# Performance work log

Hardware: AMD Instinct MI355X
Metric: run time of the kernel (lower is better)

Reference implementation:

```python
import jax, jax.numpy as jnp
import numpy as np

B, IN, H, OUT = 256, 512, 1024, 512
S, Wd, SH = 512, 256, 3          # memory_slots, memory_width, shift_range
P_READ = Wd + 2 + SH + 1         # key, beta, gate, shift(3), gamma
P_WRITE = P_READ + 2 * Wd        # + erase, add


def setup_inputs() -> dict:
    key = jax.random.key(0)
    ks = jax.random.split(key, 8)
    sc = 0.02
    return {
        "x": jax.random.normal(ks[0], (B, IN), jnp.float32),
        "W_ih": jax.random.normal(ks[1], (4 * H, IN + Wd), jnp.float32) * sc,
        "b_ih": jnp.zeros((4 * H,), jnp.float32),
        "W_hh": jax.random.normal(ks[2], (4 * H, H), jnp.float32) * sc,
        "b_hh": jnp.zeros((4 * H,), jnp.float32),
        "W_read": jax.random.normal(ks[3], (P_READ, H), jnp.float32) * sc,
        "b_read": jnp.zeros((P_READ,), jnp.float32),
        "W_write": jax.random.normal(ks[4], (P_WRITE, H), jnp.float32) * sc,
        "b_write": jnp.zeros((P_WRITE,), jnp.float32),
        "W_out": jax.random.normal(ks[5], (OUT, H + Wd), jnp.float32) * sc,
        "b_out": jnp.zeros((OUT,), jnp.float32),
        "mem_bias": jax.random.normal(ks[6], (S, Wd), jnp.float32) * sc,
    }


def _content_address(key_v, beta, memory):
    # cosine similarity of key [B,Wd] vs memory [B,S,Wd], eps=1e-8 like torch
    num = jnp.einsum('bw,bsw->bs', key_v, memory)
    kn = jnp.maximum(jnp.linalg.norm(key_v, axis=1, keepdims=True), 1e-8)
    mn = jnp.maximum(jnp.linalg.norm(memory, axis=2), 1e-8)
    sim = num / (kn * mn) * beta[:, None]
    return jax.nn.softmax(sim, axis=1)


def _address(p, prev_w, memory):
    # content_and_location addressing for a single head
    key_v = p[:, :Wd]
    beta = jax.nn.softplus(p[:, Wd])
    gate = jax.nn.sigmoid(p[:, Wd + 1])
    shift = jax.nn.softmax(p[:, Wd + 2:Wd + 2 + SH], axis=1)
    gamma = 1.0 + jax.nn.softplus(p[:, Wd + 2 + SH])
    cw = _content_address(key_v, beta, memory)
    g = gate[:, None]
    gw = g * cw + (1.0 - g) * prev_w  # interpolation gate
    # circular shift: shifted[pos] = s0*w[pos-1] + s1*w[pos] + s2*w[pos+1]
    sw = (shift[:, 0:1] * jnp.roll(gw, 1, axis=1)
          + shift[:, 1:2] * gw
          + shift[:, 2:3] * jnp.roll(gw, -1, axis=1))
    sp = sw ** gamma[:, None]  # sharpening
    return sp / (jnp.sum(sp, axis=1, keepdims=True) + 1e-6)


def reference(x, W_ih, b_ih, W_hh, b_hh, W_read, b_read, W_write, b_write, W_out, b_out, mem_bias):
    Bb = x.shape[0]
    # init_state (prev_state=None path)
    memory = jnp.broadcast_to(mem_bias[None], (Bb, S, Wd))
    w0 = jnp.zeros((Bb, S), x.dtype).at[:, 0].set(1.0)
    rv = jnp.zeros((Bb, Wd), x.dtype)
    h = jnp.zeros((Bb, H), x.dtype)
    c = jnp.zeros((Bb, H), x.dtype)
    # LSTMCell controller
    inp = jnp.concatenate([x, rv], axis=1)
    gates = inp @ W_ih.T + b_ih + h @ W_hh.T + b_hh
    i, f, g, o = jnp.split(gates, 4, axis=1)
    c = jax.nn.sigmoid(f) * c + jax.nn.sigmoid(i) * jnp.tanh(g)
    h = jax.nn.sigmoid(o) * jnp.tanh(c)
    # read head addressing (1 head)
    rp = h @ W_read.T + b_read
    read_w = _address(rp, w0, memory)
    # write head addressing + erase/add (1 head)
    wp = h @ W_write.T + b_write
    write_w = _address(wp, w0, memory)
    erase = jax.nn.sigmoid(wp[:, P_READ:P_READ + Wd])
    add = jnp.tanh(wp[:, P_READ + Wd:])
    memory = memory * (1.0 - write_w[:, :, None] * erase[:, None, :]) + write_w[:, :, None] * add[:, None, :]
    # read after write
    rv = jnp.einsum('bsw,bs->bw', memory, read_w)
    out = jnp.concatenate([h, rv], axis=1) @ W_out.T + b_out
    return out
```

## Files before the change

### kernel.cpp

```cpp
#include <hip/hip_runtime.h>
#include <hip/hip_bf16.h>
#include <math.h>

#define BB   256
#define INW  512
#define HH   1024
#define OUTW 512
#define SS   512
#define WD   256
#define P_READ  262
#define P_WRITE 774
#define RW_LD   1056
#define W_OFF   272

typedef __attribute__((ext_vector_type(8))) short bf16x8;
typedef __attribute__((ext_vector_type(4))) float f32x4;

__device__ __forceinline__ float sigmoidf(float x) { return 1.f / (1.f + expf(-x)); }
__device__ __forceinline__ float softplusf(float x) { return (x > 20.f) ? x : log1pf(expf(x)); }
__device__ __forceinline__ unsigned short f2b(float f) {
    union { float f; unsigned u; } c; c.f = f;
    return (unsigned short)((c.u + 0x7FFFu + ((c.u >> 16) & 1u)) >> 16);
}
__device__ __forceinline__ void st_bf4(__hip_bfloat16* d, float a, float b, float c, float e) {
    ushort4 u; u.x = f2b(a); u.y = f2b(b); u.z = f2b(c); u.w = f2b(e);
    *reinterpret_cast<ushort4*>(d) = u;
}
__device__ __forceinline__ float wave_sum(float v) {
    #pragma unroll
    for (int off = 32; off > 0; off >>= 1) v += __shfl_down(v, off, 64);
    return v;
}

#define N_WIH (3072*512)
#define N_WRW (RW_LD*1024)
#define N_WO  (512*1280)
#define N_X   (256*512)
#define N_MB  (512*256)
#define N_MT  (256*512)
#define N_BIA 3072
#define N_BRW RW_LD
#define N_TOT (N_WIH+N_WRW+N_WO+N_X+N_MB+N_MT+N_BIA+N_BRW)
#define NB_CVT ((N_TOT/4 + 255) / 256)

__global__ __launch_bounds__(256)
void convert_all(const float* __restrict__ W_ih, const float* __restrict__ b_ih,
                 const float* __restrict__ b_hh,
                 const float* __restrict__ W_read, const float* __restrict__ b_read,
                 const float* __restrict__ W_write, const float* __restrict__ b_write,
                 const float* __restrict__ W_out, const float* __restrict__ x,
                 const float* __restrict__ mem,
                 __hip_bfloat16* __restrict__ Wih_c, __hip_bfloat16* __restrict__ Wrw_p,
                 __hip_bfloat16* __restrict__ Wo_b, __hip_bfloat16* __restrict__ x_b,
                 __hip_bfloat16* __restrict__ mem_b, __hip_bfloat16* __restrict__ memT_b,
                 float* __restrict__ bias_c, float* __restrict__ bias_rw,
                 float* __restrict__ mem_norm)
{
    if (blockIdx.x >= NB_CVT) {
        __shared__ float red[4];
        int s = blockIdx.x - NB_CVT;
        float v = mem[(size_t)s * WD + threadIdx.x];
        float vv = wave_sum(v * v);
        if ((threadIdx.x & 63) == 0) red[threadIdx.x >> 6] = vv;
        __syncthreads();
        if (threadIdx.x == 0)
            mem_norm[s] = fmaxf(sqrtf(red[0] + red[1] + red[2] + red[3]), 1e-8f);
        return;
    }
    long i = ((long)blockIdx.x * 256 + threadIdx.x) * 4;
    if (i >= N_TOT) return;
    if (i < N_WIH) {
        int r = (int)(i >> 9), c = (int)(i & 511);
        int sr = r < 1024 ? r : r + 1024;
        float4 v = *reinterpret_cast<const float4*>(W_ih + (size_t)sr * 768 + c);
        st_bf4(Wih_c + i, v.x, v.y, v.z, v.w);
        return;
    }
    i -= N_WIH;
    if (i < N_WRW) {
        int r = (int)(i >> 10), c = (int)(i & 1023);
        float4 v = make_float4(0.f, 0.f, 0.f, 0.f);
        if (r < W_OFF) { if (r < P_READ) v = *reinterpret_cast<const float4*>(W_read + (size_t)r * 1024 + c); }
        else { int wr = r - W_OFF; if (wr < P_WRITE) v = *reinterpret_cast<const float4*>(W_write + (size_t)wr * 1024 + c); }
        st_bf4(Wrw_p + i, v.x, v.y, v.z, v.w);
        return;
    }
    i -= N_WRW;
    if (i < N_WO) {
        float4 v = *reinterpret_cast<const float4*>(W_out + i);
        st_bf4(Wo_b + i, v.x, v.y, v.z, v.w);
        return;
    }
    i -= N_WO;
    if (i < N_X) {
        float4 v = *reinterpret_cast<const float4*>(x + i);
        st_bf4(x_b + i, v.x, v.y, v.z, v.w);
        return;
    }
    i -= N_X;
    if (i < N_MB) {
        float4 v = *reinterpret_cast<const float4*>(mem + i);
        st_bf4(mem_b + i, v.x, v.y, v.z, v.w);
        return;
    }
    i -= N_MB;
    if (i < N_MT) {
        int w = (int)(i >> 9), s = (int)(i & 511);
        st_bf4(memT_b + i, mem[(size_t)s * 256 + w], mem[(size_t)(s + 1) * 256 + w],
               mem[(size_t)(s + 2) * 256 + w], mem[(size_t)(s + 3) * 256 + w]);
        return;
    }
    i -= N_MT;
    if (i < N_BIA) {
        #pragma unroll
        for (int u = 0; u < 4; ++u) {
            long r = i + u;
            long sr = r < 1024 ? r : r + 1024;
            bias_c[r] = b_ih[sr] + b_hh[sr];
        }
        return;
    }
    i -= N_BIA;
    {
        #pragma unroll
        for (int u = 0; u < 4; ++u) {
            long r = i + u;
            float v = 0.f;
            if (r < W_OFF) { if (r < P_READ) v = b_read[r]; }
            else { long wr = r - W_OFF; if (wr < P_WRITE) v = b_write[wr]; }
            bias_rw[r] = v;
        }
    }
}

__global__ __launch_bounds__(64)
void gemm_gates(const __hip_bfloat16* __restrict__ x_b,
                const __hip_bfloat16* __restrict__ Wih_c,
                const float* __restrict__ bias_c,
                __hip_bfloat16* __restrict__ h_b)
{
    const int l = threadIdx.x;
    const int bn = blockIdx.x * 16;
    const int bm = blockIdx.y * 16;
    const int r = l & 15, q = l >> 4;
    const __hip_bfloat16* ap = x_b + (size_t)(bm + r) * INW + q * 8;
    const __hip_bfloat16* bi = Wih_c + (size_t)(bn + r) * INW + q * 8;
    const __hip_bfloat16* bg = bi + (size_t)1024 * INW;
    const __hip_bfloat16* bo = bi + (size_t)2048 * INW;
    f32x4 ai = {0.f,0.f,0.f,0.f}, ag = ai, ao = ai;
    #pragma unroll
    for (int k = 0; k < INW; k += 32) {
        bf16x8 a = *reinterpret_cast<const bf16x8*>(ap + k);
        ai = __builtin_amdgcn_mfma_f32_16x16x32_bf16(a, *reinterpret_cast<const bf16x8*>(bi + k), ai, 0, 0, 0);
        ag = __builtin_amdgcn_mfma_f32_16x16x32_bf16(a, *reinterpret_cast<const bf16x8*>(bg + k), ag, 0, 0, 0);
        ao = __builtin_amdgcn_mfma_f32_16x16x32_bf16(a, *reinterpret_cast<const bf16x8*>(bo + k), ao, 0, 0, 0);
    }
    const int j = bn + r;
    const float bii = bias_c[j], big = bias_c[1024 + j], bio = bias_c[2048 + j];
    #pragma unroll
    for (int jj = 0; jj < 4; ++jj) {
        int b = bm + q * 4 + jj;
        float c = sigmoidf(ai[jj] + bii) * tanhf(ag[jj] + big);
        h_b[(size_t)b * HH + j] = __float2bfloat16(sigmoidf(ao[jj] + bio) * tanhf(c));
    }
}

__global__ __launch_bounds__(64)
void gemm_dual(const __hip_bfloat16* __restrict__ h_b,
               const __hip_bfloat16* __restrict__ Wrw_p,
               const __hip_bfloat16* __restrict__ Wo_b,
               const float* __restrict__ bias_rw, const float* __restrict__ b_out,
               float* __restrict__ rpwp, float* __restrict__ out,
               __hip_bfloat16* __restrict__ keys)
{
    const int bid = blockIdx.x;
    const int lane = threadIdx.x;
    const int r = lane & 15, q = lane >> 4;
    int bm, bn, ldb;
    const __hip_bfloat16* B;
    if (bid < 1056) { int nt = bid % 66, mt = bid / 66; bm = mt * 16; bn = nt * 16; B = Wrw_p; ldb = HH; }
    else { int o = bid - 1056; int nt = o & 31, mt = o >> 5; bm = mt * 16; bn = nt * 16; B = Wo_b; ldb = 1280; }

    const __hip_bfloat16* ap = h_b + (size_t)(bm + r) * HH + q * 8;
    const __hip_bfloat16* bp = B + (size_t)(bn + r) * ldb + q * 8;
    f32x4 a0 = {0.f,0.f,0.f,0.f}, a1 = a0;
    #pragma unroll 8
    for (int k = 0; k < 512; k += 32) {
        a0 = __builtin_amdgcn_mfma_f32_16x16x32_bf16(
            *reinterpret_cast<const bf16x8*>(ap + k),
            *reinterpret_cast<const bf16x8*>(bp + k), a0, 0, 0, 0);
        a1 = __builtin_amdgcn_mfma_f32_16x16x32_bf16(
            *reinterpret_cast<const bf16x8*>(ap + 512 + k),
            *reinterpret_cast<const bf16x8*>(bp + 512 + k), a1, 0, 0, 0);
    }
    const int col = bn + r;
    if (bid < 1056) {
        const float bv = bias_rw[col];
        #pragma unroll
        for (int j = 0; j < 4; ++j) {
            int m = bm + q * 4 + j;
            float v = a0[j] + a1[j] + bv;
            rpwp[(size_t)m * RW_LD + col] = v;
            if (col < WD)
                keys[(size_t)m * WD + col] = __float2bfloat16(v);
            else if (col >= W_OFF && col < W_OFF + WD)
                keys[(size_t)(256 + m) * WD + (col - W_OFF)] = __float2bfloat16(v);
        }
    } else {
        const float bv = b_out[col];
        #pragma unroll
        for (int j = 0; j < 4; ++j) {
            int m = bm + q * 4 + j;
            out[(size_t)m * OUTW + col] = a0[j] + a1[j] + bv;
        }
    }
}

__global__ __launch_bounds__(64)
void gemm_num(const __hip_bfloat16* __restrict__ keys,
              const __hip_bfloat16* __restrict__ mem_b,
              const float* __restrict__ mem_norm,
              float* __restrict__ numd)
{
    const int l = threadIdx.x;
    const int bn = blockIdx.x * 16;
    const int bm = blockIdx.y * 16;
    const int r = l & 15, q = l >> 4;
    const __hip_bfloat16* ap = keys + (size_t)(bm + r) * WD + q * 8;
    const __hip_bfloat16* bp = mem_b + (size_t)(bn + r) * WD + q * 8;
    f32x4 acc = {0.f,0.f,0.f,0.f};
    #pragma unroll
    for (int k = 0; k < WD; k += 32)
        acc = __builtin_amdgcn_mfma_f32_16x16x32_bf16(
            *reinterpret_cast<const bf16x8*>(ap + k),
            *reinterpret_cast<const bf16x8*>(bp + k), acc, 0, 0, 0);
    const int col = bn + r;
    const float inv = 1.f / mem_norm[col];
    #pragma unroll
    for (int j = 0; j < 4; ++j)
        numd[(size_t)(bm + q * 4 + j) * SS + col] = acc[j] * inv;
}

__device__ __forceinline__ void redpair_sum(float& a, float& b, volatile float* redA, volatile float* redB) {
    #pragma unroll
    for (int off = 32; off > 0; off >>= 1) { a += __shfl_down(a, off, 64); b += __shfl_down(b, off, 64); }
    int wid = threadIdx.x >> 6;
    __syncthreads();
    if ((threadIdx.x & 63) == 0) { redA[wid] = a; redB[wid] = b; }
    __syncthreads();
    a = redA[0]+redA[1]+redA[2]+redA[3]+redA[4]+redA[5]+redA[6]+redA[7];
    b = redB[0]+redB[1]+redB[2]+redB[3]+redB[4]+redB[5]+redB[6]+redB[7];
}
__device__ __forceinline__ void redpair_max(float& a, float& b, volatile float* redA, volatile float* redB) {
    #pragma unroll
    for (int off = 32; off > 0; off >>= 1) { a = fmaxf(a, __shfl_down(a, off, 64)); b = fmaxf(b, __shfl_down(b, off, 64)); }
    int wid = threadIdx.x >> 6;
    __syncthreads();
    if ((threadIdx.x & 63) == 0) { redA[wid] = a; redB[wid] = b; }
    __syncthreads();
    a = fmaxf(fmaxf(fmaxf(redA[0],redA[1]),fmaxf(redA[2],redA[3])),fmaxf(fmaxf(redA[4],redA[5]),fmaxf(redA[6],redA[7])));
    b = fmaxf(fmaxf(fmaxf(redB[0],redB[1]),fmaxf(redB[2],redB[3])),fmaxf(fmaxf(redB[4],redB[5]),fmaxf(redB[6],redB[7])));
}

__global__ __launch_bounds__(512)
void address_fused(const float* __restrict__ rpwp, const float* __restrict__ numd,
                   __hip_bfloat16* __restrict__ A12, float* __restrict__ t3)
{
    const int b = blockIdx.x;
    const int t = threadIdx.x;
    const float* pr = rpwp + (size_t)b * RW_LD;
    const float* pw = pr + W_OFF;

    __shared__ float redA[8], redB[8];
    __shared__ float bufr[SS], bufw[SS];

    float beta_r  = softplusf(pr[WD]);
    float gate_r  = sigmoidf(pr[WD + 1]);
    float r0 = pr[WD+2], r1 = pr[WD+3], r2 = pr[WD+4];
    float rmx = fmaxf(r0, fmaxf(r1, r2));
    float re0 = expf(r0-rmx), re1 = expf(r1-rmx), re2 = expf(r2-rmx);
    float rinv = 1.f / (re0+re1+re2);
    float shr0 = re0*rinv, shr1 = re1*rinv, shr2 = re2*rinv;
    float gamma_r = 1.f + softplusf(pr[WD + 5]);

    float beta_w  = softplusf(pw[WD]);
    float gate_w  = sigmoidf(pw[WD + 1]);
    float w0 = pw[WD+2], w1 = pw[WD+3], w2 = pw[WD+4];
    float wmx = fmaxf(w0, fmaxf(w1, w2));
    float we0 = expf(w0-wmx), we1 = expf(w1-wmx), we2 = expf(w2-wmx);
    float winv = 1.f / (we0+we1+we2);
    float shw0 = we0*winv, shw1 = we1*winv, shw2 = we2*winv;
    float gamma_w = 1.f + softplusf(pw[WD + 5]);

    {
        float kv = (t < WD) ? pr[t] : pw[t - WD];
        float vv = kv * kv;
        #pragma unroll
        for (int off = 32; off > 0; off >>= 1) vv += __shfl_down(vv, off, 64);
        int wid = t >> 6;
        if ((t & 63) == 0) redA[wid] = vv;
        __syncthreads();
    }
    float knr = fmaxf(sqrtf(redA[0]+redA[1]+redA[2]+redA[3]), 1e-8f);
    float knw = fmaxf(sqrtf(redA[4]+redA[5]+redA[6]+redA[7]), 1e-8f);
    __syncthreads();

    float sim_r = numd[(size_t)b * SS + t]         / knr * beta_r;
    float sim_w = numd[(size_t)(256 + b) * SS + t] / knw * beta_w;

    float mr = sim_r, mw = sim_w;
    redpair_max(mr, mw, redA, redB);
    float exr = expf(sim_r - mr), exw = expf(sim_w - mw);
    float sr = exr, sw = exw;
    redpair_sum(sr, sw, redA, redB);
    float cwr = exr / sr, cww = exw / sw;

    float onehot = (t == 0) ? 1.f : 0.f;
    float gwr = gate_r * cwr + (1.f - gate_r) * onehot;
    float gww = gate_w * cww + (1.f - gate_w) * onehot;
    __syncthreads();
    bufr[t] = gwr; bufw[t] = gww;
    __syncthreads();

    int tm = (t + SS - 1) & (SS - 1), tp = (t + 1) & (SS - 1);
    float swr = shr0 * bufr[tm] + shr1 * gwr + shr2 * bufr[tp];
    float sww = shw0 * bufw[tm] + shw1 * gww + shw2 * bufw[tp];

    float spr = powf(fmaxf(swr, 0.f), gamma_r), spw = powf(fmaxf(sww, 0.f), gamma_w);
    float ssr = spr, ssw = spw;
    redpair_sum(ssr, ssw, redA, redB);
    float rfin = spr / (ssr + 1e-6f);
    float wfin = spw / (ssw + 1e-6f);

    float prod = rfin * wfin;
    A12[(size_t)b * SS + t] = __float2bfloat16(rfin);
    A12[(size_t)(256 + b) * SS + t] = __float2bfloat16(prod);
    float tp3 = prod, dummy = 0.f;
    redpair_sum(tp3, dummy, redA, redB);
    if (t == 0) t3[b] = tp3;
}

__global__ __launch_bounds__(64)
void gemm_t12rv(const __hip_bfloat16* __restrict__ A12,
                const __hip_bfloat16* __restrict__ memT_b,
                const float* __restrict__ rpwp, const float* __restrict__ t3,
                __hip_bfloat16* __restrict__ rv_b)
{
    const int l = threadIdx.x;
    const int bn = blockIdx.x * 16;
    const int bm = blockIdx.y * 16;
    const int r = l & 15, q = l >> 4;
    const __hip_bfloat16* a1 = A12 + (size_t)(bm + r) * SS + q * 8;
    const __hip_bfloat16* a2 = a1 + (size_t)256 * SS;
    const __hip_bfloat16* bp = memT_b + (size_t)(bn + r) * SS + q * 8;
    f32x4 acc1 = {0.f,0.f,0.f,0.f}, acc2 = acc1;
    #pragma unroll
    for (int k = 0; k < SS; k += 32) {
        bf16x8 bb = *reinterpret_cast<const bf16x8*>(bp + k);
        acc1 = __builtin_amdgcn_mfma_f32_16x16x32_bf16(*reinterpret_cast<const bf16x8*>(a1 + k), bb, acc1, 0, 0, 0);
        acc2 = __builtin_amdgcn_mfma_f32_16x16x32_bf16(*reinterpret_cast<const bf16x8*>(a2 + k), bb, acc2, 0, 0, 0);
    }
    const int w = bn + r;
    #pragma unroll
    for (int j = 0; j < 4; ++j) {
        int b = bm + q * 4 + j;
        const float* row = rpwp + (size_t)b * RW_LD;
        float e = sigmoidf(row[W_OFF + P_READ + w]);
        float a = tanhf(row[W_OFF + P_READ + WD + w]);
        float rv = acc1[j] - e * acc2[j] + a * t3[b];
        rv_b[(size_t)b * WD + w] = __float2bfloat16(rv);
    }
}

__global__ __launch_bounds__(64)
void gemm_outrv(const __hip_bfloat16* __restrict__ rv_b,
                const __hip_bfloat16* __restrict__ Wo_b,
                float* __restrict__ out)
{
    const int l = threadIdx.x;
    const int bn = blockIdx.x * 16;
    const int bm = blockIdx.y * 16;
    const int r = l & 15, q = l >> 4;
    const __hip_bfloat16* ap = rv_b + (size_t)(bm + r) * WD + q * 8;
    const __hip_bfloat16* bp = Wo_b + (size_t)(bn + r) * 1280 + 1024 + q * 8;
    f32x4 acc = {0.f,0.f,0.f,0.f};
    #pragma unroll
    for (int k = 0; k < WD; k += 32)
        acc = __builtin_amdgcn_mfma_f32_16x16x32_bf16(
            *reinterpret_cast<const bf16x8*>(ap + k),
            *reinterpret_cast<const bf16x8*>(bp + k), acc, 0, 0, 0);
    const int col = bn + r;
    #pragma unroll
    for (int j = 0; j < 4; ++j) {
        int m = bm + q * 4 + j;
        out[(size_t)m * OUTW + col] += acc[j];
    }
}

extern "C" void kernel_launch(void* const* d_in, const int* in_sizes, int n_in,
                              void* d_out, int out_size, void* d_ws, size_t ws_size,
                              hipStream_t stream)
{
    const float* x       = (const float*)d_in[0];
    const float* W_ih    = (const float*)d_in[1];
    const float* b_ih    = (const float*)d_in[2];
    const float* b_hh    = (const float*)d_in[4];
    const float* W_read  = (const float*)d_in[5];
    const float* b_read  = (const float*)d_in[6];
    const float* W_write = (const float*)d_in[7];
    const float* b_write = (const float*)d_in[8];
    const float* W_out   = (const float*)d_in[9];
    const float* b_out   = (const float*)d_in[10];
    const float* mem     = (const float*)d_in[11];

    float* ws = (float*)d_ws;
    float* rpwp     = ws;
    float* numd     = ws + 270336;
    float* bias_c   = ws + 532480;
    float* bias_rw  = ws + 535552;
    float* mem_norm = ws + 536608;
    float* t3       = ws + 537120;
    __hip_bfloat16* bfb = (__hip_bfloat16*)(ws + 537376);
    __hip_bfloat16* x_b    = bfb;
    __hip_bfloat16* Wih_c  = bfb + 131072;
    __hip_bfloat16* Wrw_p  = bfb + 1703936;
    __hip_bfloat16* Wo_b   = bfb + 2785280;
    __hip_bfloat16* mem_b  = bfb + 3440640;
    __hip_bfloat16* memT_b = bfb + 3571712;
    __hip_bfloat16* h_b    = bfb + 3702784;
    __hip_bfloat16* keys   = bfb + 3964928;
    __hip_bfloat16* A12    = bfb + 4096000;
    __hip_bfloat16* rv_b   = bfb + 4358144;
    float* out = (float*)d_out;

    convert_all<<<NB_CVT + SS, 256, 0, stream>>>(
        W_ih, b_ih, b_hh, W_read, b_read, W_write, b_write, W_out, x, mem,
        Wih_c, Wrw_p, Wo_b, x_b, mem_b, memT_b, bias_c, bias_rw, mem_norm);
    gemm_gates<<<dim3(64, 16), 64, 0, stream>>>(x_b, Wih_c, bias_c, h_b);
    gemm_dual<<<1568, 64, 0, stream>>>(h_b, Wrw_p, Wo_b, bias_rw, b_out, rpwp, out, keys);
    gemm_num<<<dim3(32, 32), 64, 0, stream>>>(keys, mem_b, mem_norm, numd);
    address_fused<<<BB, 512, 0, stream>>>(rpwp, numd, A12, t3);
    gemm_t12rv<<<dim3(16, 16), 64, 0, stream>>>(A12, memT_b, rpwp, t3, rv_b);
    gemm_outrv<<<dim3(32, 16), 64, 0, stream>>>(rv_b, Wo_b, out);
}
```

Before: 59.03 us.

## Fuse content addressing, memory norms and read-vector GEMMs into one per-batch tail kernel

Replaces gemm_num, address_fused and gemm_t12rv with a single per-batch-row kernel. It computes the key-memory dot products and memory norms with scalar FMAs straight from bf16 memory, runs the addressing, then reduces the read/write-weighted memory sums in shared memory. It also drops the transposed-memory copy, the norm blocks in convert_all, and the key and intermediate buffers. This removes two launches and global round-trips, but each of the 256 blocks re-reads the full 256 KB bf16 memory twice and does the matmuls without MFMA, so the work depends on L2 bandwidth and scalar ALU throughput.

```diff
diff --git a/kernel.cpp b/kernel.cpp
--- a/kernel.cpp
+++ b/kernel.cpp
@@ -14,10 +14,14 @@
 #define W_OFF   272
 
 typedef __attribute__((ext_vector_type(8))) short bf16x8;
+typedef __attribute__((ext_vector_type(4))) short bf16x4;
 typedef __attribute__((ext_vector_type(4))) float f32x4;
 
 __device__ __forceinline__ float sigmoidf(float x) { return 1.f / (1.f + expf(-x)); }
 __device__ __forceinline__ float softplusf(float x) { return (x > 20.f) ? x : log1pf(expf(x)); }
+__device__ __forceinline__ float b2f(short s) {
+    union { float f; unsigned u; } c; c.u = ((unsigned)(unsigned short)s) << 16; return c.f;
+}
 __device__ __forceinline__ unsigned short f2b(float f) {
     union { float f; unsigned u; } c; c.f = f;
     return (unsigned short)((c.u + 0x7FFFu + ((c.u >> 16) & 1u)) >> 16);
@@ -25,11 +29,6 @@
 __device__ __forceinline__ void st_bf4(__hip_bfloat16* d, float a, float b, float c, float e) {
     ushort4 u; u.x = f2b(a); u.y = f2b(b); u.z = f2b(c); u.w = f2b(e);
     *reinterpret_cast<ushort4*>(d) = u;
-}
-__device__ __forceinline__ float wave_sum(float v) {
-    #pragma unroll
-    for (int off = 32; off > 0; off >>= 1) v += __shfl_down(v, off, 64);
-    return v;
 }
 
 #define N_WIH (3072*512)
@@ -37,10 +36,9 @@
 #define N_WO  (512*1280)
 #define N_X   (256*512)
 #define N_MB  (512*256)
-#define N_MT  (256*512)
 #define N_BIA 3072
 #define N_BRW RW_LD
-#define N_TOT (N_WIH+N_WRW+N_WO+N_X+N_MB+N_MT+N_BIA+N_BRW)
+#define N_TOT (N_WIH+N_WRW+N_WO+N_X+N_MB+N_BIA+N_BRW)
 #define NB_CVT ((N_TOT/4 + 255) / 256)
 
 __global__ __launch_bounds__(256)
@@ -52,21 +50,9 @@
                  const float* __restrict__ mem,
                  __hip_bfloat16* __restrict__ Wih_c, __hip_bfloat16* __restrict__ Wrw_p,
                  __hip_bfloat16* __restrict__ Wo_b, __hip_bfloat16* __restrict__ x_b,
-                 __hip_bfloat16* __restrict__ mem_b, __hip_bfloat16* __restrict__ memT_b,
-                 float* __restrict__ bias_c, float* __restrict__ bias_rw,
-                 float* __restrict__ mem_norm)
-{
-    if (blockIdx.x >= NB_CVT) {
-        __shared__ float red[4];
-        int s = blockIdx.x - NB_CVT;
-        float v = mem[(size_t)s * WD + threadIdx.x];
-        float vv = wave_sum(v * v);
-        if ((threadIdx.x & 63) == 0) red[threadIdx.x >> 6] = vv;
-        __syncthreads();
-        if (threadIdx.x == 0)
-            mem_norm[s] = fmaxf(sqrtf(red[0] + red[1] + red[2] + red[3]), 1e-8f);
-        return;
-    }
+                 __hip_bfloat16* __restrict__ mem_b,
+                 float* __restrict__ bias_c, float* __restrict__ bias_rw)
+{
     long i = ((long)blockIdx.x * 256 + threadIdx.x) * 4;
     if (i >= N_TOT) return;
     if (i < N_WIH) {
@@ -104,13 +90,6 @@
         return;
     }
     i -= N_MB;
-    if (i < N_MT) {
-        int w = (int)(i >> 9), s = (int)(i & 511);
-        st_bf4(memT_b + i, mem[(size_t)s * 256 + w], mem[(size_t)(s + 1) * 256 + w],
-               mem[(size_t)(s + 2) * 256 + w], mem[(size_t)(s + 3) * 256 + w]);
-        return;
-    }
-    i -= N_MT;
     if (i < N_BIA) {
         #pragma unroll
         for (int u = 0; u < 4; ++u) {
@@ -170,8 +149,7 @@
                const __hip_bfloat16* __restrict__ Wrw_p,
                const __hip_bfloat16* __restrict__ Wo_b,
                const float* __restrict__ bias_rw, const float* __restrict__ b_out,
-               float* __restrict__ rpwp, float* __restrict__ out,
-               __hip_bfloat16* __restrict__ keys)
+               float* __restrict__ rpwp, float* __restrict__ out)
 {
     const int bid = blockIdx.x;
     const int lane = threadIdx.x;
@@ -199,12 +177,7 @@
         #pragma unroll
         for (int j = 0; j < 4; ++j) {
             int m = bm + q * 4 + j;
-            float v = a0[j] + a1[j] + bv;
-            rpwp[(size_t)m * RW_LD + col] = v;
-            if (col < WD)
-                keys[(size_t)m * WD + col] = __float2bfloat16(v);
-            else if (col >= W_OFF && col < W_OFF + WD)
-                keys[(size_t)(256 + m) * WD + (col - W_OFF)] = __float2bfloat16(v);
+            rpwp[(size_t)m * RW_LD + col] = a0[j] + a1[j] + bv;
         }
     } else {
         const float bv = b_out[col];
@@ -216,31 +189,6 @@
     }
 }
 
-__global__ __launch_bounds__(64)
-void gemm_num(const __hip_bfloat16* __restrict__ keys,
-              const __hip_bfloat16* __restrict__ mem_b,
-              const float* __restrict__ mem_norm,
-              float* __restrict__ numd)
-{
-    const int l = threadIdx.x;
-    const int bn = blockIdx.x * 16;
-    const int bm = blockIdx.y * 16;
-    const int r = l & 15, q = l >> 4;
-    const __hip_bfloat16* ap = keys + (size_t)(bm + r) * WD + q * 8;
-    const __hip_bfloat16* bp = mem_b + (size_t)(bn + r) * WD + q * 8;
-    f32x4 acc = {0.f,0.f,0.f,0.f};
-    #pragma unroll
-    for (int k = 0; k < WD; k += 32)
-        acc = __builtin_amdgcn_mfma_f32_16x16x32_bf16(
-            *reinterpret_cast<const bf16x8*>(ap + k),
-            *reinterpret_cast<const bf16x8*>(bp + k), acc, 0, 0, 0);
-    const int col = bn + r;
-    const float inv = 1.f / mem_norm[col];
-    #pragma unroll
-    for (int j = 0; j < 4; ++j)
-        numd[(size_t)(bm + q * 4 + j) * SS + col] = acc[j] * inv;
-}
-
 __device__ __forceinline__ void redpair_sum(float& a, float& b, volatile float* redA, volatile float* redB) {
     #pragma unroll
     for (int off = 32; off > 0; off >>= 1) { a += __shfl_down(a, off, 64); b += __shfl_down(b, off, 64); }
@@ -263,112 +211,144 @@
 }
 
 __global__ __launch_bounds__(512)
-void address_fused(const float* __restrict__ rpwp, const float* __restrict__ numd,
-                   __hip_bfloat16* __restrict__ A12, float* __restrict__ t3)
-{
+void tail_kernel(const float* __restrict__ rpwp,
+                 const __hip_bfloat16* __restrict__ mem_b,
+                 __hip_bfloat16* __restrict__ rv_b)
+{
+    __shared__ float redA[8], redB[8];
+    __shared__ __align__(16) float s_keyr[256], s_keyw[256];
+    __shared__ float s_simr[512], s_simw[512], s_nrm[512];
+    __shared__ float bufr[512], bufw[512];
+    __shared__ float s_rw[512], s_pw[512];
+    __shared__ float s_p1[8][256], s_p2[8][256];
+
     const int b = blockIdx.x;
     const int t = threadIdx.x;
-    const float* pr = rpwp + (size_t)b * RW_LD;
-    const float* pw = pr + W_OFF;
-
-    __shared__ float redA[8], redB[8];
-    __shared__ float bufr[SS], bufw[SS];
-
-    float beta_r  = softplusf(pr[WD]);
-    float gate_r  = sigmoidf(pr[WD + 1]);
-    float r0 = pr[WD+2], r1 = pr[WD+3], r2 = pr[WD+4];
-    float rmx = fmaxf(r0, fmaxf(r1, r2));
-    float re0 = expf(r0-rmx), re1 = expf(r1-rmx), re2 = expf(r2-rmx);
-    float rinv = 1.f / (re0+re1+re2);
-    float shr0 = re0*rinv, shr1 = re1*rinv, shr2 = re2*rinv;
-    float gamma_r = 1.f + softplusf(pr[WD + 5]);
-
-    float beta_w  = softplusf(pw[WD]);
-    float gate_w  = sigmoidf(pw[WD + 1]);
-    float w0 = pw[WD+2], w1 = pw[WD+3], w2 = pw[WD+4];
-    float wmx = fmaxf(w0, fmaxf(w1, w2));
-    float we0 = expf(w0-wmx), we1 = expf(w1-wmx), we2 = expf(w2-wmx);
-    float winv = 1.f / (we0+we1+we2);
-    float shw0 = we0*winv, shw1 = we1*winv, shw2 = we2*winv;
-    float gamma_w = 1.f + softplusf(pw[WD + 5]);
-
+    const int lane = t & 63;
+    const int w = t >> 6;
+    const float* pr  = rpwp + (size_t)b * RW_LD;
+    const float* pw2 = pr + W_OFF;
+
+    float kv = (t < 256) ? pr[t] : pw2[t - 256];
+    if (t < 256) s_keyr[t] = kv; else s_keyw[t - 256] = kv;
     {
-        float kv = (t < WD) ? pr[t] : pw[t - WD];
         float vv = kv * kv;
         #pragma unroll
         for (int off = 32; off > 0; off >>= 1) vv += __shfl_down(vv, off, 64);
-        int wid = t >> 6;
-        if ((t & 63) == 0) redA[wid] = vv;
+        if (lane == 0) redA[w] = vv;
+    }
+    __syncthreads();
+    const float knr = fmaxf(sqrtf(redA[0]+redA[1]+redA[2]+redA[3]), 1e-8f);
+    const float knw = fmaxf(sqrtf(redA[4]+redA[5]+redA[6]+redA[7]), 1e-8f);
+
+    {
+        const int half = lane >> 5;
+        const int l32 = lane & 31;
+        float kr8[8], kw8[8];
+        #pragma unroll
+        for (int e = 0; e < 8; ++e) { kr8[e] = s_keyr[l32 * 8 + e]; kw8[e] = s_keyw[l32 * 8 + e]; }
+        for (int j = 0; j < 32; ++j) {
+            int s = w * 64 + 2 * j + half;
+            bf16x8 m8 = *reinterpret_cast<const bf16x8*>(mem_b + (size_t)s * WD + l32 * 8);
+            float nr = 0.f, nw = 0.f, nn = 0.f;
+            #pragma unroll
+            for (int e = 0; e < 8; ++e) {
+                float mv = b2f(m8[e]);
+                nr += kr8[e] * mv; nw += kw8[e] * mv; nn += mv * mv;
+            }
+            #pragma unroll
+            for (int off = 1; off < 32; off <<= 1) {
+                nr += __shfl_xor(nr, off, 64);
+                nw += __shfl_xor(nw, off, 64);
+                nn += __shfl_xor(nn, off, 64);
+            }
+            if (l32 == 0) {
+                s_simr[s] = nr; s_simw[s] = nw;
+                s_nrm[s] = fmaxf(sqrtf(nn), 1e-8f);
+            }
+        }
+    }
+    __syncthreads();
+
+    float t3v;
+    {
+        float beta_r  = softplusf(pr[WD]);
+        float gate_r  = sigmoidf(pr[WD + 1]);
+        float r0 = pr[WD+2], r1 = pr[WD+3], r2 = pr[WD+4];
+        float rmx = fmaxf(r0, fmaxf(r1, r2));
+        float re0 = expf(r0-rmx), re1 = expf(r1-rmx), re2 = expf(r2-rmx);
+        float rinv = 1.f / (re0+re1+re2);
+        float shr0 = re0*rinv, shr1 = re1*rinv, shr2 = re2*rinv;
+        float gamma_r = 1.f + softplusf(pr[WD + 5]);
+
+        float beta_w  = softplusf(pw2[WD]);
+        float gate_w  = sigmoidf(pw2[WD + 1]);
+        float w0 = pw2[WD+2], w1 = pw2[WD+3], w2 = pw2[WD+4];
+        float wmx = fmaxf(w0, fmaxf(w1, w2));
+        float we0 = expf(w0-wmx), we1 = expf(w1-wmx), we2 = expf(w2-wmx);
+        float winv = 1.f / (we0+we1+we2);
+        float shw0 = we0*winv, shw1 = we1*winv, shw2 = we2*winv;
+        float gamma_w = 1.f + softplusf(pw2[WD + 5]);
+
+        float ninv = 1.f / s_nrm[t];
+        float sim_r = s_simr[t] * ninv / knr * beta_r;
+        float sim_w = s_simw[t] * ninv / knw * beta_w;
+
+        float mr = sim_r, mw = sim_w;
+        redpair_max(mr, mw, redA, redB);
+        float exr = expf(sim_r - mr), exw = expf(sim_w - mw);
+        float sr = exr, sw = exw;
+        redpair_sum(sr, sw, redA, redB);
+        float cwr = exr / sr, cww = exw / sw;
+
+        float onehot = (t == 0) ? 1.f : 0.f;
+        float gwr = gate_r * cwr + (1.f - gate_r) * onehot;
+        float gww = gate_w * cww + (1.f - gate_w) * onehot;
         __syncthreads();
-    }
-    float knr = fmaxf(sqrtf(redA[0]+redA[1]+redA[2]+redA[3]), 1e-8f);
-    float knw = fmaxf(sqrtf(redA[4]+redA[5]+redA[6]+redA[7]), 1e-8f);
-    __syncthreads();
-
-    float sim_r = numd[(size_t)b * SS + t]         / knr * beta_r;
-    float sim_w = numd[(size_t)(256 + b) * SS + t] / knw * beta_w;
-
-    float mr = sim_r, mw = sim_w;
-    redpair_max(mr, mw, redA, redB);
-    float exr = expf(sim_r - mr), exw = expf(sim_w - mw);
-    float sr = exr, sw = exw;
-    redpair_sum(sr, sw, redA, redB);
-    float cwr = exr / sr, cww = exw / sw;
-
-    float onehot = (t == 0) ? 1.f : 0.f;
-    float gwr = gate_r * cwr + (1.f - gate_r) * onehot;
-    float gww = gate_w * cww + (1.f - gate_w) * onehot;
-    __syncthreads();
-    bufr[t] = gwr; bufw[t] = gww;
-    __syncthreads();
-
-    int tm = (t + SS - 1) & (SS - 1), tp = (t + 1) & (SS - 1);
-    float swr = shr0 * bufr[tm] + shr1 * gwr + shr2 * bufr[tp];
-    float sww = shw0 * bufw[tm] + shw1 * gww + shw2 * bufw[tp];
-
-    float spr = powf(fmaxf(swr, 0.f), gamma_r), spw = powf(fmaxf(sww, 0.f), gamma_w);
-    float ssr = spr, ssw = spw;
-    redpair_sum(ssr, ssw, redA, redB);
-    float rfin = spr / (ssr + 1e-6f);
-    float wfin = spw / (ssw + 1e-6f);
-
-    float prod = rfin * wfin;
-    A12[(size_t)b * SS + t] = __float2bfloat16(rfin);
-    A12[(size_t)(256 + b) * SS + t] = __float2bfloat16(prod);
-    float tp3 = prod, dummy = 0.f;
-    redpair_sum(tp3, dummy, redA, redB);
-    if (t == 0) t3[b] = tp3;
-}
-
-__global__ __launch_bounds__(64)
-void gemm_t12rv(const __hip_bfloat16* __restrict__ A12,
-                const __hip_bfloat16* __restrict__ memT_b,
-                const float* __restrict__ rpwp, const float* __restrict__ t3,
-                __hip_bfloat16* __restrict__ rv_b)
-{
-    const int l = threadIdx.x;
-    const int bn = blockIdx.x * 16;
-    const int bm = blockIdx.y * 16;
-    const int r = l & 15, q = l >> 4;
-    const __hip_bfloat16* a1 = A12 + (size_t)(bm + r) * SS + q * 8;
-    const __hip_bfloat16* a2 = a1 + (size_t)256 * SS;
-    const __hip_bfloat16* bp = memT_b + (size_t)(bn + r) * SS + q * 8;
-    f32x4 acc1 = {0.f,0.f,0.f,0.f}, acc2 = acc1;
-    #pragma unroll
-    for (int k = 0; k < SS; k += 32) {
-        bf16x8 bb = *reinterpret_cast<const bf16x8*>(bp + k);
-        acc1 = __builtin_amdgcn_mfma_f32_16x16x32_bf16(*reinterpret_cast<const bf16x8*>(a1 + k), bb, acc1, 0, 0, 0);
-        acc2 = __builtin_amdgcn_mfma_f32_16x16x32_bf16(*reinterpret_cast<const bf16x8*>(a2 + k), bb, acc2, 0, 0, 0);
-    }
-    const int w = bn + r;
-    #pragma unroll
-    for (int j = 0; j < 4; ++j) {
-        int b = bm + q * 4 + j;
-        const float* row = rpwp + (size_t)b * RW_LD;
-        float e = sigmoidf(row[W_OFF + P_READ + w]);
-        float a = tanhf(row[W_OFF + P_READ + WD + w]);
-        float rv = acc1[j] - e * acc2[j] + a * t3[b];
-        rv_b[(size_t)b * WD + w] = __float2bfloat16(rv);
+        bufr[t] = gwr; bufw[t] = gww;
+        __syncthreads();
+
+        int tm = (t + SS - 1) & (SS - 1), tp = (t + 1) & (SS - 1);
+        float swr = shr0 * bufr[tm] + shr1 * gwr + shr2 * bufr[tp];
+        float sww = shw0 * bufw[tm] + shw1 * gww + shw2 * bufw[tp];
+
+        float spr = powf(fmaxf(swr, 0.f), gamma_r), spw = powf(fmaxf(sww, 0.f), gamma_w);
+        float ssr = spr, ssw = spw;
+        redpair_sum(ssr, ssw, redA, redB);
+        float rfin = spr / (ssr + 1e-6f);
+        float wfin = spw / (ssw + 1e-6f);
+        float prod = rfin * wfin;
+
+        s_rw[t] = rfin; s_pw[t] = prod;
+        float tp3 = prod, dmy = 0.f;
+        redpair_sum(tp3, dmy, redA, redB);
+        t3v = tp3;
+    }
+    __syncthreads();
+
+    {
+        const int wcol = lane * 4;
+        float a1_0=0.f,a1_1=0.f,a1_2=0.f,a1_3=0.f;
+        float a2_0=0.f,a2_1=0.f,a2_2=0.f,a2_3=0.f;
+        const int s0 = w * 64;
+        for (int s = s0; s < s0 + 64; ++s) {
+            bf16x4 m4 = *reinterpret_cast<const bf16x4*>(mem_b + (size_t)s * WD + wcol);
+            float rw = s_rw[s], pwv = s_pw[s];
+            float m0 = b2f(m4[0]), m1 = b2f(m4[1]), m2 = b2f(m4[2]), m3 = b2f(m4[3]);
+            a1_0 += rw * m0; a1_1 += rw * m1; a1_2 += rw * m2; a1_3 += rw * m3;
+            a2_0 += pwv * m0; a2_1 += pwv * m1; a2_2 += pwv * m2; a2_3 += pwv * m3;
+        }
+        s_p1[w][wcol] = a1_0; s_p1[w][wcol+1] = a1_1; s_p1[w][wcol+2] = a1_2; s_p1[w][wcol+3] = a1_3;
+        s_p2[w][wcol] = a2_0; s_p2[w][wcol+1] = a2_1; s_p2[w][wcol+2] = a2_2; s_p2[w][wcol+3] = a2_3;
+    }
+    __syncthreads();
+    if (t < 256) {
+        float t1 = 0.f, t2 = 0.f;
+        #pragma unroll
+        for (int ww = 0; ww < 8; ++ww) { t1 += s_p1[ww][t]; t2 += s_p2[ww][t]; }
+        float e = sigmoidf(pw2[P_READ + t]);
+        float a = tanhf(pw2[P_READ + WD + t]);
+        rv_b[(size_t)b * WD + t] = __float2bfloat16(t1 - e * t2 + a * t3v);
     }
 }
 
@@ -415,31 +395,23 @@
 
     float* ws = (float*)d_ws;
     float* rpwp     = ws;
-    float* numd     = ws + 270336;
-    float* bias_c   = ws + 532480;
-    float* bias_rw  = ws + 535552;
-    float* mem_norm = ws + 536608;
-    float* t3       = ws + 537120;
-    __hip_bfloat16* bfb = (__hip_bfloat16*)(ws + 537376);
+    float* bias_c   = ws + 270336;
+    float* bias_rw  = ws + 273408;
+    __hip_bfloat16* bfb = (__hip_bfloat16*)(ws + 274464);
     __hip_bfloat16* x_b    = bfb;
     __hip_bfloat16* Wih_c  = bfb + 131072;
     __hip_bfloat16* Wrw_p  = bfb + 1703936;
     __hip_bfloat16* Wo_b   = bfb + 2785280;
     __hip_bfloat16* mem_b  = bfb + 3440640;
-    __hip_bfloat16* memT_b = bfb + 3571712;
-    __hip_bfloat16* h_b    = bfb + 3702784;
-    __hip_bfloat16* keys   = bfb + 3964928;
-    __hip_bfloat16* A12    = bfb + 4096000;
-    __hip_bfloat16* rv_b   = bfb + 4358144;
+    __hip_bfloat16* h_b    = bfb + 3571712;
+    __hip_bfloat16* rv_b   = bfb + 3833856;
     float* out = (float*)d_out;
 
-    convert_all<<<NB_CVT + SS, 256, 0, stream>>>(
+    convert_all<<<NB_CVT, 256, 0, stream>>>(
         W_ih, b_ih, b_hh, W_read, b_read, W_write, b_write, W_out, x, mem,
-        Wih_c, Wrw_p, Wo_b, x_b, mem_b, memT_b, bias_c, bias_rw, mem_norm);
+        Wih_c, Wrw_p, Wo_b, x_b, mem_b, bias_c, bias_rw);
     gemm_gates<<<dim3(64, 16), 64, 0, stream>>>(x_b, Wih_c, bias_c, h_b);
-    gemm_dual<<<1568, 64, 0, stream>>>(h_b, Wrw_p, Wo_b, bias_rw, b_out, rpwp, out, keys);
-    gemm_num<<<dim3(32, 32), 64, 0, stream>>>(keys, mem_b, mem_norm, numd);
-    address_fused<<<BB, 512, 0, stream>>>(rpwp, numd, A12, t3);
-    gemm_t12rv<<<dim3(16, 16), 64, 0, stream>>>(A12, memT_b, rpwp, t3, rv_b);
+    gemm_dual<<<1568, 64, 0, stream>>>(h_b, Wrw_p, Wo_b, bias_rw, b_out, rpwp, out);
+    tail_kernel<<<BB, 512, 0, stream>>>(rpwp, mem_b, rv_b);
     gemm_outrv<<<dim3(32, 16), 64, 0, stream>>>(rv_b, Wo_b, out);
 }
```

After: 76.85 us. +30.2%, slower.

## Fuse content GEMM, addressing, read GEMM and output GEMM into one per-batch kernel

Applied to the files above, without the earlier changes.

Replaces four kernels (num GEMM, addressing, t12/rv GEMM, out-rv GEMM) with a single per-batch-row tail kernel that keeps the intermediates in shared memory. The cost it targets is launch overhead and the global round trips for numd, A12, t3 and rv. Keys are interleaved per batch row so each block can load its two key rows. In exchange, each block runs MFMAs with only 2 useful rows out of 16, which wastes most of the matrix throughput. Each block also re-reads all of mem_b, memT_b and the Wo slice, so L2 traffic rises.

```diff
diff --git a/kernel.cpp b/kernel.cpp
--- a/kernel.cpp
+++ b/kernel.cpp
@@ -202,9 +202,9 @@
             float v = a0[j] + a1[j] + bv;
             rpwp[(size_t)m * RW_LD + col] = v;
             if (col < WD)
-                keys[(size_t)m * WD + col] = __float2bfloat16(v);
+                keys[(size_t)(2 * m) * WD + col] = __float2bfloat16(v);
             else if (col >= W_OFF && col < W_OFF + WD)
-                keys[(size_t)(256 + m) * WD + (col - W_OFF)] = __float2bfloat16(v);
+                keys[(size_t)(2 * m + 1) * WD + (col - W_OFF)] = __float2bfloat16(v);
         }
     } else {
         const float bv = b_out[col];
@@ -214,31 +214,6 @@
             out[(size_t)m * OUTW + col] = a0[j] + a1[j] + bv;
         }
     }
-}
-
-__global__ __launch_bounds__(64)
-void gemm_num(const __hip_bfloat16* __restrict__ keys,
-              const __hip_bfloat16* __restrict__ mem_b,
-              const float* __restrict__ mem_norm,
-              float* __restrict__ numd)
-{
-    const int l = threadIdx.x;
-    const int bn = blockIdx.x * 16;
-    const int bm = blockIdx.y * 16;
-    const int r = l & 15, q = l >> 4;
-    const __hip_bfloat16* ap = keys + (size_t)(bm + r) * WD + q * 8;
-    const __hip_bfloat16* bp = mem_b + (size_t)(bn + r) * WD + q * 8;
-    f32x4 acc = {0.f,0.f,0.f,0.f};
-    #pragma unroll
-    for (int k = 0; k < WD; k += 32)
-        acc = __builtin_amdgcn_mfma_f32_16x16x32_bf16(
-            *reinterpret_cast<const bf16x8*>(ap + k),
-            *reinterpret_cast<const bf16x8*>(bp + k), acc, 0, 0, 0);
-    const int col = bn + r;
-    const float inv = 1.f / mem_norm[col];
-    #pragma unroll
-    for (int j = 0; j < 4; ++j)
-        numd[(size_t)(bm + q * 4 + j) * SS + col] = acc[j] * inv;
 }
 
 __device__ __forceinline__ void redpair_sum(float& a, float& b, volatile float* redA, volatile float* redB) {
@@ -263,137 +238,162 @@
 }
 
 __global__ __launch_bounds__(512)
-void address_fused(const float* __restrict__ rpwp, const float* __restrict__ numd,
-                   __hip_bfloat16* __restrict__ A12, float* __restrict__ t3)
+void tail_kernel(const float* __restrict__ rpwp, const float* __restrict__ mem_norm,
+                 const __hip_bfloat16* __restrict__ keys,
+                 const __hip_bfloat16* __restrict__ mem_b,
+                 const __hip_bfloat16* __restrict__ memT_b,
+                 const __hip_bfloat16* __restrict__ Wo_b,
+                 float* __restrict__ out)
 {
+    __shared__ float redA[8], redB[8];
+    __shared__ float s_num[2][520];
+    __shared__ __hip_bfloat16 s_a12[2][512];
+    __shared__ float s_t12[2][264];
+    __shared__ __hip_bfloat16 s_rv[264];
+    __shared__ float bufr[512], bufw[512];
+
     const int b = blockIdx.x;
     const int t = threadIdx.x;
-    const float* pr = rpwp + (size_t)b * RW_LD;
-    const float* pw = pr + W_OFF;
-
-    __shared__ float redA[8], redB[8];
-    __shared__ float bufr[SS], bufw[SS];
-
-    float beta_r  = softplusf(pr[WD]);
-    float gate_r  = sigmoidf(pr[WD + 1]);
-    float r0 = pr[WD+2], r1 = pr[WD+3], r2 = pr[WD+4];
-    float rmx = fmaxf(r0, fmaxf(r1, r2));
-    float re0 = expf(r0-rmx), re1 = expf(r1-rmx), re2 = expf(r2-rmx);
-    float rinv = 1.f / (re0+re1+re2);
-    float shr0 = re0*rinv, shr1 = re1*rinv, shr2 = re2*rinv;
-    float gamma_r = 1.f + softplusf(pr[WD + 5]);
-
-    float beta_w  = softplusf(pw[WD]);
-    float gate_w  = sigmoidf(pw[WD + 1]);
-    float w0 = pw[WD+2], w1 = pw[WD+3], w2 = pw[WD+4];
-    float wmx = fmaxf(w0, fmaxf(w1, w2));
-    float we0 = expf(w0-wmx), we1 = expf(w1-wmx), we2 = expf(w2-wmx);
-    float winv = 1.f / (we0+we1+we2);
-    float shw0 = we0*winv, shw1 = we1*winv, shw2 = we2*winv;
-    float gamma_w = 1.f + softplusf(pw[WD + 5]);
-
-    {
-        float kv = (t < WD) ? pr[t] : pw[t - WD];
+    const int lane = t & 63;
+    const int w = t >> 6;
+    const int r = lane & 15, q = lane >> 4;
+    const float* pr  = rpwp + (size_t)b * RW_LD;
+    const float* pw2 = pr + W_OFF;
+
+    {
+        float kv = (t < 256) ? pr[t] : pw2[t - 256];
         float vv = kv * kv;
         #pragma unroll
         for (int off = 32; off > 0; off >>= 1) vv += __shfl_down(vv, off, 64);
-        int wid = t >> 6;
-        if ((t & 63) == 0) redA[wid] = vv;
+        if (lane == 0) redA[w] = vv;
+    }
+    __syncthreads();
+    const float knr = fmaxf(sqrtf(redA[0]+redA[1]+redA[2]+redA[3]), 1e-8f);
+    const float knw = fmaxf(sqrtf(redA[4]+redA[5]+redA[6]+redA[7]), 1e-8f);
+    __syncthreads();
+
+    {
+        const int ar = (r < 2) ? r : 0;
+        const __hip_bfloat16* ap = keys + (size_t)(2 * b + ar) * WD + q * 8;
+        bf16x8 afr[8];
+        #pragma unroll
+        for (int k8 = 0; k8 < 8; ++k8)
+            afr[k8] = *reinterpret_cast<const bf16x8*>(ap + k8 * 32);
+        #pragma unroll
+        for (int i = 0; i < 4; ++i) {
+            const int bn = (w + i * 8) * 16;
+            const __hip_bfloat16* bp = mem_b + (size_t)(bn + r) * WD + q * 8;
+            f32x4 acc = {0.f,0.f,0.f,0.f};
+            #pragma unroll
+            for (int k8 = 0; k8 < 8; ++k8)
+                acc = __builtin_amdgcn_mfma_f32_16x16x32_bf16(
+                    afr[k8], *reinterpret_cast<const bf16x8*>(bp + k8 * 32), acc, 0, 0, 0);
+            if (q == 0) { s_num[0][bn + r] = acc[0]; s_num[1][bn + r] = acc[1]; }
+        }
+    }
+    __syncthreads();
+
+    float t3v;
+    {
+        float beta_r  = softplusf(pr[WD]);
+        float gate_r  = sigmoidf(pr[WD + 1]);
+        float r0 = pr[WD+2], r1 = pr[WD+3], r2 = pr[WD+4];
+        float rmx = fmaxf(r0, fmaxf(r1, r2));
+        float re0 = expf(r0-rmx), re1 = expf(r1-rmx), re2 = expf(r2-rmx);
+        float rinv = 1.f / (re0+re1+re2);
+        float shr0 = re0*rinv, shr1 = re1*rinv, shr2 = re2*rinv;
+        float gamma_r = 1.f + softplusf(pr[WD + 5]);
+
+        float beta_w  = softplusf(pw2[WD]);
+        float gate_w  = sigmoidf(pw2[WD + 1]);
+        float w0 = pw2[WD+2], w1 = pw2[WD+3], w2 = pw2[WD+4];
+        float wmx = fmaxf(w0, fmaxf(w1, w2));
+        float we0 = expf(w0-wmx), we1 = expf(w1-wmx), we2 = expf(w2-wmx);
+        float winv = 1.f / (we0+we1+we2);
+        float shw0 = we0*winv, shw1 = we1*winv, shw2 = we2*winv;
+        float gamma_w = 1.f + softplusf(pw2[WD + 5]);
+
+        float ninv = 1.f / mem_norm[t];
+        float sim_r = s_num[0][t] * ninv / knr * beta_r;
+        float sim_w = s_num[1][t] * ninv / knw * beta_w;
+
+        float mr = sim_r, mw = sim_w;
+        redpair_max(mr, mw, redA, redB);
+        float exr = expf(sim_r - mr), exw = expf(sim_w - mw);
+        float sr = exr, sw = exw;
+        redpair_sum(sr, sw, redA, redB);
+        float cwr = exr / sr, cww = exw / sw;
+
+        float onehot = (t == 0) ? 1.f : 0.f;
+        float gwr = gate_r * cwr + (1.f - gate_r) * onehot;
+        float gww = gate_w * cww + (1.f - gate_w) * onehot;
         __syncthreads();
-    }
-    float knr = fmaxf(sqrtf(redA[0]+redA[1]+redA[2]+redA[3]), 1e-8f);
-    float knw = fmaxf(sqrtf(redA[4]+redA[5]+redA[6]+redA[7]), 1e-8f);
-    __syncthreads();
-
-    float sim_r = numd[(size_t)b * SS + t]         / knr * beta_r;
-    float sim_w = numd[(size_t)(256 + b) * SS + t] / knw * beta_w;
-
-    float mr = sim_r, mw = sim_w;
-    redpair_max(mr, mw, redA, redB);
-    float exr = expf(sim_r - mr), exw = expf(sim_w - mw);
-    float sr = exr, sw = exw;
-    redpair_sum(sr, sw, redA, redB);
-    float cwr = exr / sr, cww = exw / sw;
-
-    float onehot = (t == 0) ? 1.f : 0.f;
-    float gwr = gate_r * cwr + (1.f - gate_r) * onehot;
-    float gww = gate_w * cww + (1.f - gate_w) * onehot;
-    __syncthreads();
-    bufr[t] = gwr; bufw[t] = gww;
-    __syncthreads();
-
-    int tm = (t + SS - 1) & (SS - 1), tp = (t + 1) & (SS - 1);
-    float swr = shr0 * bufr[tm] + shr1 * gwr + shr2 * bufr[tp];
-    float sww = shw0 * bufw[tm] + shw1 * gww + shw2 * bufw[tp];
-
-    float spr = powf(fmaxf(swr, 0.f), gamma_r), spw = powf(fmaxf(sww, 0.f), gamma_w);
-    float ssr = spr, ssw = spw;
-    redpair_sum(ssr, ssw, redA, redB);
-    float rfin = spr / (ssr + 1e-6f);
-    float wfin = spw / (ssw + 1e-6f);
-
-    float prod = rfin * wfin;
-    A12[(size_t)b * SS + t] = __float2bfloat16(rfin);
-    A12[(size_t)(256 + b) * SS + t] = __float2bfloat16(prod);
-    float tp3 = prod, dummy = 0.f;
-    redpair_sum(tp3, dummy, redA, redB);
-    if (t == 0) t3[b] = tp3;
-}
-
-__global__ __launch_bounds__(64)
-void gemm_t12rv(const __hip_bfloat16* __restrict__ A12,
-                const __hip_bfloat16* __restrict__ memT_b,
-                const float* __restrict__ rpwp, const float* __restrict__ t3,
-                __hip_bfloat16* __restrict__ rv_b)
-{
-    const int l = threadIdx.x;
-    const int bn = blockIdx.x * 16;
-    const int bm = blockIdx.y * 16;
-    const int r = l & 15, q = l >> 4;
-    const __hip_bfloat16* a1 = A12 + (size_t)(bm + r) * SS + q * 8;
-    const __hip_bfloat16* a2 = a1 + (size_t)256 * SS;
-    const __hip_bfloat16* bp = memT_b + (size_t)(bn + r) * SS + q * 8;
-    f32x4 acc1 = {0.f,0.f,0.f,0.f}, acc2 = acc1;
-    #pragma unroll
-    for (int k = 0; k < SS; k += 32) {
-        bf16x8 bb = *reinterpret_cast<const bf16x8*>(bp + k);
-        acc1 = __builtin_amdgcn_mfma_f32_16x16x32_bf16(*reinterpret_cast<const bf16x8*>(a1 + k), bb, acc1, 0, 0, 0);
-        acc2 = __builtin_amdgcn_mfma_f32_16x16x32_bf16(*reinterpret_cast<const bf16x8*>(a2 + k), bb, acc2, 0, 0, 0);
-    }
-    const int w = bn + r;
-    #pragma unroll
-    for (int j = 0; j < 4; ++j) {
-        int b = bm + q * 4 + j;
-        const float* row = rpwp + (size_t)b * RW_LD;
-        float e = sigmoidf(row[W_OFF + P_READ + w]);
-        float a = tanhf(row[W_OFF + P_READ + WD + w]);
-        float rv = acc1[j] - e * acc2[j] + a * t3[b];
-        rv_b[(size_t)b * WD + w] = __float2bfloat16(rv);
-    }
-}
-
-__global__ __launch_bounds__(64)
-void gemm_outrv(const __hip_bfloat16* __restrict__ rv_b,
-                const __hip_bfloat16* __restrict__ Wo_b,
-                float* __restrict__ out)
-{
-    const int l = threadIdx.x;
-    const int bn = blockIdx.x * 16;
-    const int bm = blockIdx.y * 16;
-    const int r = l & 15, q = l >> 4;
-    const __hip_bfloat16* ap = rv_b + (size_t)(bm + r) * WD + q * 8;
-    const __hip_bfloat16* bp = Wo_b + (size_t)(bn + r) * 1280 + 1024 + q * 8;
-    f32x4 acc = {0.f,0.f,0.f,0.f};
-    #pragma unroll
-    for (int k = 0; k < WD; k += 32)
-        acc = __builtin_amdgcn_mfma_f32_16x16x32_bf16(
-            *reinterpret_cast<const bf16x8*>(ap + k),
-            *reinterpret_cast<const bf16x8*>(bp + k), acc, 0, 0, 0);
-    const int col = bn + r;
-    #pragma unroll
-    for (int j = 0; j < 4; ++j) {
-        int m = bm + q * 4 + j;
-        out[(size_t)m * OUTW + col] += acc[j];
+        bufr[t] = gwr; bufw[t] = gww;
+        __syncthreads();
+
+        int tm = (t + SS - 1) & (SS - 1), tp = (t + 1) & (SS - 1);
+        float swr = shr0 * bufr[tm] + shr1 * gwr + shr2 * bufr[tp];
+        float sww = shw0 * bufw[tm] + shw1 * gww + shw2 * bufw[tp];
+
+        float spr = powf(fmaxf(swr, 0.f), gamma_r), spw = powf(fmaxf(sww, 0.f), gamma_w);
+        float ssr = spr, ssw = spw;
+        redpair_sum(ssr, ssw, redA, redB);
+        float rfin = spr / (ssr + 1e-6f);
+        float wfin = spw / (ssw + 1e-6f);
+        float prod = rfin * wfin;
+
+        s_a12[0][t] = __float2bfloat16(rfin);
+        s_a12[1][t] = __float2bfloat16(prod);
+        float tp3 = prod, dmy = 0.f;
+        redpair_sum(tp3, dmy, redA, redB);
+        t3v = tp3;
+    }
+    __syncthreads();
+
+    {
+        const int ar = (r < 2) ? r : 0;
+        const __hip_bfloat16* ap = &s_a12[ar][q * 8];
+        #pragma unroll
+        for (int i = 0; i < 2; ++i) {
+            const int bn = (w + i * 8) * 16;
+            const __hip_bfloat16* bp = memT_b + (size_t)(bn + r) * SS + q * 8;
+            f32x4 acc = {0.f,0.f,0.f,0.f};
+            #pragma unroll
+            for (int k = 0; k < SS; k += 32)
+                acc = __builtin_amdgcn_mfma_f32_16x16x32_bf16(
+                    *reinterpret_cast<const bf16x8*>(ap + k),
+                    *reinterpret_cast<const bf16x8*>(bp + k), acc, 0, 0, 0);
+            if (q == 0) { s_t12[0][bn + r] = acc[0]; s_t12[1][bn + r] = acc[1]; }
+        }
+    }
+    __syncthreads();
+
+    if (t < 256) {
+        float t1 = s_t12[0][t], t2 = s_t12[1][t];
+        float e = sigmoidf(pw2[P_READ + t]);
+        float a = tanhf(pw2[P_READ + WD + t]);
+        s_rv[t] = __float2bfloat16(t1 - e * t2 + a * t3v);
+    }
+    __syncthreads();
+
+    {
+        const __hip_bfloat16* ap = &s_rv[q * 8];
+        bf16x8 afr[8];
+        #pragma unroll
+        for (int k8 = 0; k8 < 8; ++k8)
+            afr[k8] = *reinterpret_cast<const bf16x8*>(ap + k8 * 32);
+        #pragma unroll
+        for (int i = 0; i < 4; ++i) {
+            const int bn = (w + i * 8) * 16;
+            const __hip_bfloat16* bp = Wo_b + (size_t)(bn + r) * 1280 + 1024 + q * 8;
+            f32x4 acc = {0.f,0.f,0.f,0.f};
+            #pragma unroll
+            for (int k8 = 0; k8 < 8; ++k8)
+                acc = __builtin_amdgcn_mfma_f32_16x16x32_bf16(
+                    afr[k8], *reinterpret_cast<const bf16x8*>(bp + k8 * 32), acc, 0, 0, 0);
+            if (q == 0)
+                out[(size_t)b * OUTW + bn + r] += acc[0];
+        }
     }
 }
 
@@ -415,12 +415,10 @@
 
     float* ws = (float*)d_ws;
     float* rpwp     = ws;
-    float* numd     = ws + 270336;
-    float* bias_c   = ws + 532480;
-    float* bias_rw  = ws + 535552;
-    float* mem_norm = ws + 536608;
-    float* t3       = ws + 537120;
-    __hip_bfloat16* bfb = (__hip_bfloat16*)(ws + 537376);
+    float* bias_c   = ws + 270336;
+    float* bias_rw  = ws + 273408;
+    float* mem_norm = ws + 274464;
+    __hip_bfloat16* bfb = (__hip_bfloat16*)(ws + 274976);
     __hip_bfloat16* x_b    = bfb;
     __hip_bfloat16* Wih_c  = bfb + 131072;
     __hip_bfloat16* Wrw_p  = bfb + 1703936;
@@ -429,8 +427,6 @@
     __hip_bfloat16* memT_b = bfb + 3571712;
     __hip_bfloat16* h_b    = bfb + 3702784;
     __hip_bfloat16* keys   = bfb + 3964928;
-    __hip_bfloat16* A12    = bfb + 4096000;
-    __hip_bfloat16* rv_b   = bfb + 4358144;
     float* out = (float*)d_out;
 
     convert_all<<<NB_CVT + SS, 256, 0, stream>>>(
@@ -438,8 +434,5 @@
         Wih_c, Wrw_p, Wo_b, x_b, mem_b, memT_b, bias_c, bias_rw, mem_norm);
     gemm_gates<<<dim3(64, 16), 64, 0, stream>>>(x_b, Wih_c, bias_c, h_b);
     gemm_dual<<<1568, 64, 0, stream>>>(h_b, Wrw_p, Wo_b, bias_rw, b_out, rpwp, out, keys);
-    gemm_num<<<dim3(32, 32), 64, 0, stream>>>(keys, mem_b, mem_norm, numd);
-    address_fused<<<BB, 512, 0, stream>>>(rpwp, numd, A12, t3);
-    gemm_t12rv<<<dim3(16, 16), 64, 0, stream>>>(A12, memT_b, rpwp, t3, rv_b);
-    gemm_outrv<<<dim3(32, 16), 64, 0, stream>>>(rv_b, Wo_b, out);
-}
+    tail_kernel<<<BB, 512, 0, stream>>>(rpwp, mem_norm, keys, mem_b, memT_b, Wo_b, out);
+}
```

Result: slower. 70.91 us (+20.1%).
